# Kernel tuning notes

Measured on AMD Instinct MI355X. Metric: run time of the kernel, lower is better.

## Reference

```python
import jax, jax.numpy as jnp
import numpy as np

EPS = 1e-5

def conv1x1(x, w, b):
    # x: [B,C,H,W], w: [O,C], b: [O]
    return jnp.einsum('oc,bchw->bohw', w, x) + b[None, :, None, None]

def mean_variance_norm(feat):
    # per-(batch,channel) stats over spatial dims; torch.var default is unbiased (ddof=1)
    b, c = feat.shape[:2]
    flat = feat.reshape(b, c, -1)
    mean = jnp.mean(flat, axis=2)[:, :, None, None]
    std = jnp.sqrt(jnp.var(flat, axis=2, ddof=1) + EPS)[:, :, None, None]
    return (feat - mean) / std

def setup_inputs() -> dict:
    key = jax.random.key(0)
    ks = jax.random.split(key, 10)
    B, C, H, W = 4, 256, 64, 64
    sc = 1.0 / np.sqrt(C)
    return {
        'content': jax.random.normal(ks[0], (B, C, H, W), jnp.float32),
        'style': jax.random.normal(ks[1], (B, C, H, W), jnp.float32),
        'content_key': jax.random.normal(ks[2], (B, C, H, W), jnp.float32),
        'style_key': jax.random.normal(ks[3], (B, C, H, W), jnp.float32),
        'f_w': jax.random.normal(ks[4], (C, C), jnp.float32) * sc,
        'f_b': jax.random.normal(ks[5], (C,), jnp.float32) * 0.01,
        'g_w': jax.random.normal(ks[6], (C, C), jnp.float32) * sc,
        'g_b': jax.random.normal(ks[7], (C,), jnp.float32) * 0.01,
        'h_w': jax.random.normal(ks[8], (C, C), jnp.float32) * sc,
        'h_b': jax.random.normal(ks[9], (C,), jnp.float32) * 0.01,
    }

def reference(content, style, content_key, style_key, f_w, f_b, g_w, g_b, h_w, h_b):
    Fq = conv1x1(content_key, f_w, f_b)   # [B,C,Hc,Wc]
    G = conv1x1(style_key, g_w, g_b)      # [B,C,Hs,Ws]
    Hv = conv1x1(style, h_w, h_b)         # [B,C,Hs,Ws]
    b, c, h, w = Fq.shape
    hw_c = h * w
    hw_s = G.shape[2] * G.shape[3]
    Fm = Fq.reshape(b, c, hw_c).transpose(0, 2, 1)       # [B,Nq,C]
    Gm = G.reshape(b, c, hw_s)                            # [B,C,Nk]
    style_flat = Hv.reshape(b, c, hw_s).transpose(0, 2, 1)  # [B,Nk,C]
    S = jax.nn.softmax(jnp.einsum('bqc,bck->bqk', Fm, Gm), axis=-1)  # [B,Nq,Nk]
    mean = jnp.einsum('bqk,bkc->bqc', S, style_flat)
    second = jnp.einsum('bqk,bkc->bqc', S, style_flat ** 2)
    std = jnp.sqrt(jax.nn.relu(second - mean ** 2))
    mean = mean.reshape(b, h, w, c).transpose(0, 3, 1, 2)
    std = std.reshape(b, h, w, c).transpose(0, 3, 1, 2)
    return std * mean_variance_norm(content) + mean
```

## Files before the change

### kernel.cpp

```cpp
#include <hip/hip_runtime.h>
#include <math.h>

#define NSP 4096
#define CD  256
#define LOG2E 1.44269504f

typedef _Float16 half8 __attribute__((ext_vector_type(8)));
typedef _Float16 half4v __attribute__((ext_vector_type(4)));
typedef float f32x4 __attribute__((ext_vector_type(4)));
typedef unsigned int u32;

#define VMCNT(n) asm volatile("s_waitcnt vmcnt(" #n ")" ::: "memory")
#define LGKM0    asm volatile("s_waitcnt lgkmcnt(0)" ::: "memory")

__device__ __forceinline__ void gl16(const void* g, void* l) {
    __builtin_amdgcn_global_load_lds((const __attribute__((address_space(1))) u32*)g,
                                     (__attribute__((address_space(3))) u32*)l, 16, 0, 0);
}

template<int MODE>
__global__ __launch_bounds__(256, 2) void conv_kernel(
    const float* __restrict__ W, const float* __restrict__ bias,
    const float* __restrict__ Xall, _Float16* __restrict__ Yh, _Float16* __restrict__ Yl)
{
    const int b = blockIdx.z;
    const float* X = Xall + (size_t)b * CD * NSP;
    _Float16* Yhb = Yh + (size_t)b * CD * NSP * (MODE == 2 ? 2 : 1);
    _Float16* Ylb = (MODE == 2) ? nullptr : Yl + (size_t)b * CD * NSP;
    __shared__ float Ws[16][128];
    __shared__ float Xs[16][128];
    const int t = threadIdx.x;
    const int tx = t & 15, ty = t >> 4;
    const int m0 = blockIdx.y * 128, n0 = blockIdx.x * 128;
    float acc[8][8];
#pragma unroll
    for (int i = 0; i < 8; ++i)
#pragma unroll
        for (int j = 0; j < 8; ++j) acc[i][j] = 0.f;

    for (int k0 = 0; k0 < CD; k0 += 16) {
        __syncthreads();
        {
            int m = t >> 1, k = (t & 1) * 8;
            float4 w0 = *reinterpret_cast<const float4*>(&W[(size_t)(m0 + m) * CD + k0 + k]);
            float4 w1 = *reinterpret_cast<const float4*>(&W[(size_t)(m0 + m) * CD + k0 + k + 4]);
            Ws[k + 0][m] = w0.x; Ws[k + 1][m] = w0.y; Ws[k + 2][m] = w0.z; Ws[k + 3][m] = w0.w;
            Ws[k + 4][m] = w1.x; Ws[k + 5][m] = w1.y; Ws[k + 6][m] = w1.z; Ws[k + 7][m] = w1.w;
        }
        {
            int k = t >> 4, n = (t & 15) * 8;
            *reinterpret_cast<float4*>(&Xs[k][n]) =
                *reinterpret_cast<const float4*>(&X[(size_t)(k0 + k) * NSP + n0 + n]);
            *reinterpret_cast<float4*>(&Xs[k][n + 4]) =
                *reinterpret_cast<const float4*>(&X[(size_t)(k0 + k) * NSP + n0 + n + 4]);
        }
        __syncthreads();
#pragma unroll
        for (int k = 0; k < 16; ++k) {
            float a[8], bb[8];
            float4 a0 = *reinterpret_cast<const float4*>(&Ws[k][ty * 8]);
            float4 a1 = *reinterpret_cast<const float4*>(&Ws[k][ty * 8 + 4]);
            float4 b0 = *reinterpret_cast<const float4*>(&Xs[k][tx * 4]);
            float4 b1 = *reinterpret_cast<const float4*>(&Xs[k][64 + tx * 4]);
            a[0]=a0.x; a[1]=a0.y; a[2]=a0.z; a[3]=a0.w;
            a[4]=a1.x; a[5]=a1.y; a[6]=a1.z; a[7]=a1.w;
            bb[0]=b0.x; bb[1]=b0.y; bb[2]=b0.z; bb[3]=b0.w;
            bb[4]=b1.x; bb[5]=b1.y; bb[6]=b1.z; bb[7]=b1.w;
#pragma unroll
            for (int i = 0; i < 8; ++i)
#pragma unroll
                for (int j = 0; j < 8; ++j) acc[i][j] = fmaf(a[i], bb[j], acc[i][j]);
        }
    }
    float bv[8];
#pragma unroll
    for (int i = 0; i < 8; ++i) bv[i] = bias[m0 + ty * 8 + i];

    if (MODE == 0) {
#pragma unroll
        for (int jj = 0; jj < 8; ++jj) {
            int n = n0 + ((jj < 4) ? (tx * 4 + jj) : (64 + tx * 4 + (jj - 4)));
            half4v h0, h1, l0, l1;
#pragma unroll
            for (int i = 0; i < 4; ++i) {
                float y0 = (acc[i][jj] + bv[i]) * LOG2E;
                _Float16 hh0 = (_Float16)y0; h0[i] = hh0; l0[i] = (_Float16)(y0 - (float)hh0);
                float y1 = (acc[i + 4][jj] + bv[i + 4]) * LOG2E;
                _Float16 hh1 = (_Float16)y1; h1[i] = hh1; l1[i] = (_Float16)(y1 - (float)hh1);
            }
            size_t off = (size_t)n * CD + m0 + ty * 8;
            *reinterpret_cast<half4v*>(&Yhb[off])     = h0;
            *reinterpret_cast<half4v*>(&Yhb[off + 4]) = h1;
            *reinterpret_cast<half4v*>(&Ylb[off])     = l0;
            *reinterpret_cast<half4v*>(&Ylb[off + 4]) = l1;
        }
    } else if (MODE == 1) {
#pragma unroll
        for (int jj = 0; jj < 8; ++jj) {
            int n = n0 + ((jj < 4) ? (tx * 4 + jj) : (64 + tx * 4 + (jj - 4)));
            int tile = n >> 5, key = n & 31;
            int g = (m0 + ty * 8) >> 3;
            size_t base = (size_t)tile * 8192 + (size_t)key * 256
                        + ((((g * 16)) ^ ((key & 7) << 4)) >> 1);
            half4v h0, h1, l0, l1;
#pragma unroll
            for (int i = 0; i < 4; ++i) {
                float y0 = acc[i][jj] + bv[i];
                _Float16 hh0 = (_Float16)y0; h0[i] = hh0; l0[i] = (_Float16)(y0 - (float)hh0);
                float y1 = acc[i + 4][jj] + bv[i + 4];
                _Float16 hh1 = (_Float16)y1; h1[i] = hh1; l1[i] = (_Float16)(y1 - (float)hh1);
            }
            *reinterpret_cast<half4v*>(&Yhb[base])     = h0;
            *reinterpret_cast<half4v*>(&Yhb[base + 4]) = h1;
            *reinterpret_cast<half4v*>(&Ylb[base])     = l0;
            *reinterpret_cast<half4v*>(&Ylb[base + 4]) = l1;
        }
    } else {
#pragma unroll
        for (int i = 0; i < 8; ++i) {
            int ch = m0 + ty * 8 + i;
            int sw = (ch & 7) << 4;
#pragma unroll
            for (int grp = 0; grp < 2; ++grp) {
                int n = n0 + grp * 64 + tx * 4;
                int tile = n >> 5, kin = n & 31;
                int g4 = kin >> 3, pos0 = kin & 7;
                half4v hv, lv;
#pragma unroll
                for (int j = 0; j < 4; ++j) {
                    float y = acc[i][grp * 4 + j] + bv[i];
                    _Float16 hh = (_Float16)y; hv[j] = hh; lv[j] = (_Float16)(y - (float)hh);
                }
                size_t rowb = (size_t)tile * 16384 + (size_t)ch * 64;
                int bh = (g4 * 16 + pos0 * 2) ^ sw;
                int bl = (64 + g4 * 16 + pos0 * 2) ^ sw;
                *reinterpret_cast<half4v*>(&Yhb[rowb + (bh >> 1)]) = hv;
                *reinterpret_cast<half4v*>(&Yhb[rowb + (bl >> 1)]) = lv;
            }
        }
    }
}

#define KB_OFF 0
#define VB_OFF 65536
#define PB_OFF 131072
#define RM_OFF 139264
#define SMEM_BYTES 139776

__global__ __launch_bounds__(512, 2) void attn_kernel(
    const _Float16* __restrict__ Qh_g, const _Float16* __restrict__ Ql_g,
    const _Float16* __restrict__ Kh_g, const _Float16* __restrict__ Kl_g,
    const _Float16* __restrict__ Vhl_g,
    float* __restrict__ Mout, float* __restrict__ Sout)
{
    extern __shared__ char smem[];
    const int tid = threadIdx.x;
    const int lane = tid & 63;
    const int w = tid >> 6;
    const int g4 = lane >> 4;
    const int l15 = lane & 15;
    const int qf = w & 3;
    const int kf = w >> 2;

    const int bid = blockIdx.x;
    const int b = (bid & 7) >> 1;
    const int qb = ((bid >> 3) << 1) | (bid & 1);
    const int q0 = qb * 64;

    const size_t bNC = (size_t)b * NSP * CD;
    const _Float16* Qhb = Qh_g + bNC;
    const _Float16* Qlb = Ql_g + bNC;
    const _Float16* Khb = Kh_g + bNC;
    const _Float16* Klb = Kl_g + bNC;
    const _Float16* Vb  = Vhl_g + bNC * 2;

    const int qrow = q0 + qf * 16 + l15;
    half8 qh[8], ql[8];
#pragma unroll
    for (int ks = 0; ks < 8; ++ks) {
        qh[ks] = *reinterpret_cast<const half8*>(Qhb + (size_t)qrow * CD + ks * 32 + g4 * 8);
        ql[ks] = *reinterpret_cast<const half8*>(Qlb + (size_t)qrow * CD + ks * 32 + g4 * 8);
    }

    auto stageK = [&](int t, int buf) {
        const _Float16* sh = Khb + (size_t)t * 8192 + w * 1024 + lane * 8;
        const _Float16* sl = Klb + (size_t)t * 8192 + w * 1024 + lane * 8;
        char* d = smem + KB_OFF + buf * 32768 + w * 2048;
        gl16(sh,       d);
        gl16(sh + 512, d + 1024);
        gl16(sl,       d + 16384);
        gl16(sl + 512, d + 16384 + 1024);
    };
    auto stageV = [&](int t, int buf) {
        const _Float16* s = Vb + (size_t)t * 16384 + w * 2048 + lane * 8;
        char* d = smem + VB_OFF + buf * 32768 + w * 4096;
        gl16(s,        d);
        gl16(s + 512,  d + 1024);
        gl16(s + 1024, d + 2048);
        gl16(s + 1536, d + 3072);
    };

    stageK(0, 0); stageV(0, 0); stageK(1, 1); stageV(1, 1);

    f32x4 accM[2][4], accS[2][4];
#pragma unroll
    for (int m = 0; m < 2; ++m)
#pragma unroll
        for (int nf = 0; nf < 4; ++nf) {
            accM[m][nf] = (f32x4){0.f, 0.f, 0.f, 0.f};
            accS[m][nf] = (f32x4){0.f, 0.f, 0.f, 0.f};
        }
    float mrun = -3.0e38f, lrun = 0.f;

    half8 ones8;
#pragma unroll
    for (int e = 0; e < 8; ++e) ones8[e] = (_Float16)1.f;

    const int key = kf * 16 + l15;
    const int ksw = (key & 7) << 4;

    for (int t = 0; t < 128; ++t) {
        const int buf = t & 1;

        if (t < 127) { VMCNT(8); } else { VMCNT(0); }
        LGKM0;
        __builtin_amdgcn_s_barrier();
        __builtin_amdgcn_sched_barrier(0);

        half8 vh8A[2], vl8A[2], wh8A[2], wl8A[2];
#pragma unroll
        for (int m = 0; m < 2; ++m) {
            int ch = w * 32 + m * 16 + l15;
            const char* vrow = smem + VB_OFF + buf * 32768 + ch * 128;
            int sw = (ch & 7) << 4;
            half8 vh8 = *reinterpret_cast<const half8*>(vrow + ((g4 * 16) ^ sw));
            half8 vl8 = *reinterpret_cast<const half8*>(vrow + ((64 + g4 * 16) ^ sw));
            vh8A[m] = vh8; vl8A[m] = vl8;
            half8 wh8, wl8;
#pragma unroll
            for (int e = 0; e < 8; ++e) {
                float v = (float)vh8[e] + (float)vl8[e];
                float wv = v * v;
                _Float16 hh = (_Float16)wv;
                wh8[e] = hh; wl8[e] = (_Float16)(wv - (float)hh);
            }
            wh8A[m] = wh8; wl8A[m] = wl8;
        }

        const char* krow = smem + KB_OFF + buf * 32768 + key * 512;
        f32x4 s = (f32x4){0.f, 0.f, 0.f, 0.f};
        __builtin_amdgcn_s_setprio(1);
#pragma unroll
        for (int ks = 0; ks < 8; ++ks) {
            int off = ((ks * 4 + g4) * 16) ^ ksw;
            half8 bh = *reinterpret_cast<const half8*>(krow + off);
            half8 bl = *reinterpret_cast<const half8*>(krow + 16384 + off);
            s = __builtin_amdgcn_mfma_f32_16x16x32_f16(qh[ks], bh, s, 0, 0, 0);
            s = __builtin_amdgcn_mfma_f32_16x16x32_f16(qh[ks], bl, s, 0, 0, 0);
            s = __builtin_amdgcn_mfma_f32_16x16x32_f16(ql[ks], bh, s, 0, 0, 0);
        }
        __builtin_amdgcn_s_setprio(0);

        f32x4 rmax = s;
#pragma unroll
        for (int mk = 1; mk <= 8; mk <<= 1)
#pragma unroll
            for (int e = 0; e < 4; ++e) rmax[e] = fmaxf(rmax[e], __shfl_xor(rmax[e], mk));
        if (l15 == 0)
            *reinterpret_cast<f32x4*>(smem + RM_OFF + kf * 256 + (qf * 16 + g4 * 4) * 4) = rmax;

        LGKM0;
        __builtin_amdgcn_s_barrier();
        __builtin_amdgcn_sched_barrier(0);

        if (t + 2 < 128) stageK(t + 2, buf);

        const float* rmf = (const float*)(smem + RM_OFF);
        float rm01 = fmaxf(rmf[lane], rmf[64 + lane]);
        bool upd = rm01 > mrun + 8.f;
        float sc = upd ? __builtin_amdgcn_exp2f(mrun - rm01) : 1.f;
        if (upd) mrun = rm01;

#pragma unroll
        for (int e = 0; e < 4; ++e) {
            int q_e = qf * 16 + g4 * 4 + e;
            float m_e = __shfl(mrun, q_e);
            float p = __builtin_amdgcn_exp2f(s[e] - m_e);
            _Float16 hp = (_Float16)p;
            *reinterpret_cast<_Float16*>(smem + PB_OFF + q_e * 128 + ((key * 2) ^ ((q_e & 7) << 4))) = hp;
        }

        if (__ballot(sc < 1.f)) {
#pragma unroll
            for (int nf = 0; nf < 4; ++nf) {
                float scn = __shfl(sc, nf * 16 + l15);
#pragma unroll
                for (int m = 0; m < 2; ++m)
#pragma unroll
                    for (int e = 0; e < 4; ++e) { accM[m][nf][e] *= scn; accS[m][nf][e] *= scn; }
            }
        }

        LGKM0;
        __builtin_amdgcn_s_barrier();
        __builtin_amdgcn_sched_barrier(0);

        half8 pb[4];
#pragma unroll
        for (int nf = 0; nf < 4; ++nf) {
            int q = nf * 16 + l15;
            pb[nf] = *reinterpret_cast<const half8*>(smem + PB_OFF + q * 128 + ((g4 * 16) ^ ((q & 7) << 4)));
        }
        f32x4 po[4];
#pragma unroll
        for (int nf = 0; nf < 4; ++nf) po[nf] = (f32x4){0.f, 0.f, 0.f, 0.f};
        __builtin_amdgcn_s_setprio(1);
#pragma unroll
        for (int nf = 0; nf < 4; ++nf)
            po[nf] = __builtin_amdgcn_mfma_f32_16x16x32_f16(ones8, pb[nf], po[nf], 0, 0, 0);
#pragma unroll
        for (int m = 0; m < 2; ++m) {
#pragma unroll
            for (int nf = 0; nf < 4; ++nf) {
                accM[m][nf] = __builtin_amdgcn_mfma_f32_16x16x32_f16(vh8A[m], pb[nf], accM[m][nf], 0, 0, 0);
                accM[m][nf] = __builtin_amdgcn_mfma_f32_16x16x32_f16(vl8A[m], pb[nf], accM[m][nf], 0, 0, 0);
                accS[m][nf] = __builtin_amdgcn_mfma_f32_16x16x32_f16(wh8A[m], pb[nf], accS[m][nf], 0, 0, 0);
                accS[m][nf] = __builtin_amdgcn_mfma_f32_16x16x32_f16(wl8A[m], pb[nf], accS[m][nf], 0, 0, 0);
            }
        }
        __builtin_amdgcn_s_setprio(0);

        float rsum = (g4 == 0) ? po[0][0] : (g4 == 1) ? po[1][0] : (g4 == 2) ? po[2][0] : po[3][0];
        lrun = lrun * sc + rsum;

        __builtin_amdgcn_sched_barrier(0);
        LGKM0;
        if (t + 2 < 128) stageV(t + 2, buf);
    }

    float inv = 1.f / lrun;
    float linv[4];
#pragma unroll
    for (int nf = 0; nf < 4; ++nf) linv[nf] = __shfl(inv, nf * 16 + l15);

#pragma unroll
    for (int m = 0; m < 2; ++m)
#pragma unroll
        for (int nf = 0; nf < 4; ++nf) {
            int qg = q0 + nf * 16 + l15;
#pragma unroll
            for (int e = 0; e < 4; ++e) {
                int ch = w * 32 + m * 16 + g4 * 4 + e;
                float mean = accM[m][nf][e] * linv[nf];
                float sec  = accS[m][nf][e] * linv[nf];
                float var = sec - mean * mean;
                float sd = sqrtf(fmaxf(var, 0.f));
                size_t off = ((size_t)b * CD + ch) * NSP + qg;
                Mout[off] = mean;
                Sout[off] = sd;
            }
        }
}

__global__ __launch_bounds__(256) void mvn_kernel(
    const float* __restrict__ content, const float* __restrict__ Mn,
    const float* __restrict__ Sd, float* __restrict__ out)
{
    __shared__ float redS[4], redSS[4];
    const int t = threadIdx.x;
    const size_t base = (size_t)blockIdx.x * NSP;
    const float4* x4 = reinterpret_cast<const float4*>(content + base);
    float s = 0.f, ss = 0.f;
    float4 xv[4];
#pragma unroll
    for (int i = 0; i < 4; ++i) {
        float4 v = x4[i * 256 + t];
        xv[i] = v;
        s  += v.x + v.y + v.z + v.w;
        ss += v.x * v.x + v.y * v.y + v.z * v.z + v.w * v.w;
    }
#pragma unroll
    for (int mk = 1; mk < 64; mk <<= 1) { s += __shfl_xor(s, mk); ss += __shfl_xor(ss, mk); }
    if ((t & 63) == 0) { redS[t >> 6] = s; redSS[t >> 6] = ss; }
    __syncthreads();
    float tot   = redS[0] + redS[1] + redS[2] + redS[3];
    float totss = redSS[0] + redSS[1] + redSS[2] + redSS[3];
    float mu  = tot * (1.f / 4096.f);
    float var = (totss - 4096.f * mu * mu) * (1.f / 4095.f);
    float rstd = 1.f / sqrtf(var + 1e-5f);
    const float4* m4 = reinterpret_cast<const float4*>(Mn + base);
    const float4* s4 = reinterpret_cast<const float4*>(Sd + base);
    float4* o4 = reinterpret_cast<float4*>(out + base);
#pragma unroll
    for (int i = 0; i < 4; ++i) {
        float4 mv = m4[i * 256 + t];
        float4 sv = s4[i * 256 + t];
        float4 v  = xv[i];
        float4 o;
        o.x = sv.x * ((v.x - mu) * rstd) + mv.x;
        o.y = sv.y * ((v.y - mu) * rstd) + mv.y;
        o.z = sv.z * ((v.z - mu) * rstd) + mv.z;
        o.w = sv.w * ((v.w - mu) * rstd) + mv.w;
        o4[i * 256 + t] = o;
    }
}

extern "C" void kernel_launch(void* const* d_in, const int* in_sizes, int n_in,
                              void* d_out, int out_size, void* d_ws, size_t ws_size,
                              hipStream_t stream)
{
    const float* content     = (const float*)d_in[0];
    const float* style       = (const float*)d_in[1];
    const float* content_key = (const float*)d_in[2];
    const float* style_key   = (const float*)d_in[3];
    const float* f_w = (const float*)d_in[4];
    const float* f_b = (const float*)d_in[5];
    const float* g_w = (const float*)d_in[6];
    const float* g_b = (const float*)d_in[7];
    const float* h_w = (const float*)d_in[8];
    const float* h_b = (const float*)d_in[9];
    float* out = (float*)d_out;

    const size_t TS = (size_t)4 * NSP * CD;
    _Float16* ws16 = (_Float16*)d_ws;
    _Float16* Qh  = ws16;
    _Float16* Ql  = ws16 + TS;
    _Float16* Kh  = ws16 + 2 * TS;
    _Float16* Kl  = ws16 + 3 * TS;
    _Float16* Vhl = ws16 + 4 * TS;
    float* Mn = (float*)(ws16 + 6 * TS);
    float* Sd = Mn + TS;

    dim3 cgrid(32, 2, 4);
    conv_kernel<0><<<cgrid, 256, 0, stream>>>(f_w, f_b, content_key, Qh, Ql);
    conv_kernel<1><<<cgrid, 256, 0, stream>>>(g_w, g_b, style_key, Kh, Kl);
    conv_kernel<2><<<cgrid, 256, 0, stream>>>(h_w, h_b, style, Vhl, Vhl);
    attn_kernel<<<dim3(256), 512, SMEM_BYTES, stream>>>(Qh, Ql, Kh, Kl, Vhl, Mn, Sd);
    mvn_kernel<<<dim3(1024), 256, 0, stream>>>(content, Mn, Sd, out);
}
```

Baseline: 571.8 us.

## Shrink attention tile to 32 queries, load V directly to registers

```diff
diff --git a/kernel.cpp b/kernel.cpp
--- a/kernel.cpp
+++ b/kernel.cpp
@@ -119,35 +119,33 @@
 #pragma unroll
         for (int i = 0; i < 8; ++i) {
             int ch = m0 + ty * 8 + i;
-            int sw = (ch & 7) << 4;
+            int wv_ = ch >> 6, mv = (ch >> 4) & 3, lv = ch & 15;
+            size_t chbase = (size_t)(wv_ * 8 + mv) * 512 + lv * 8;
 #pragma unroll
             for (int grp = 0; grp < 2; ++grp) {
                 int n = n0 + grp * 64 + tx * 4;
                 int tile = n >> 5, kin = n & 31;
-                int g4 = kin >> 3, pos0 = kin & 7;
-                half4v hv, lv;
+                int g4v = kin >> 3, pos0 = kin & 7;
+                half4v hv, lv4;
 #pragma unroll
                 for (int j = 0; j < 4; ++j) {
                     float y = acc[i][grp * 4 + j] + bv[i];
-                    _Float16 hh = (_Float16)y; hv[j] = hh; lv[j] = (_Float16)(y - (float)hh);
+                    _Float16 hh = (_Float16)y; hv[j] = hh; lv4[j] = (_Float16)(y - (float)hh);
                 }
-                size_t rowb = (size_t)tile * 16384 + (size_t)ch * 64;
-                int bh = (g4 * 16 + pos0 * 2) ^ sw;
-                int bl = (64 + g4 * 16 + pos0 * 2) ^ sw;
-                *reinterpret_cast<half4v*>(&Yhb[rowb + (bh >> 1)]) = hv;
-                *reinterpret_cast<half4v*>(&Yhb[rowb + (bl >> 1)]) = lv;
+                size_t tb = (size_t)tile * 16384 + chbase + (size_t)g4v * 128 + pos0;
+                *reinterpret_cast<half4v*>(&Yhb[tb])        = hv;
+                *reinterpret_cast<half4v*>(&Yhb[tb + 2048]) = lv4;
             }
         }
     }
 }
 
 #define KB_OFF 0
-#define VB_OFF 65536
-#define PB_OFF 131072
-#define RM_OFF 139264
-#define SMEM_BYTES 139776
-
-__global__ __launch_bounds__(512, 2) void attn_kernel(
+#define PB_OFF 65536
+#define RM_OFF 69632
+#define SMEM_BYTES 69888
+
+__global__ __launch_bounds__(256, 2) void attn_kernel(
     const _Float16* __restrict__ Qh_g, const _Float16* __restrict__ Ql_g,
     const _Float16* __restrict__ Kh_g, const _Float16* __restrict__ Kl_g,
     const _Float16* __restrict__ Vhl_g,
@@ -159,13 +157,13 @@
     const int w = tid >> 6;
     const int g4 = lane >> 4;
     const int l15 = lane & 15;
-    const int qf = w & 3;
-    const int kf = w >> 2;
+    const int kf = w & 1;
+    const int qf = w >> 1;
 
     const int bid = blockIdx.x;
     const int b = (bid & 7) >> 1;
     const int qb = ((bid >> 3) << 1) | (bid & 1);
-    const int q0 = qb * 64;
+    const int q0 = qb * 32;
 
     const size_t bNC = (size_t)b * NSP * CD;
     const _Float16* Qhb = Qh_g + bNC;
@@ -183,30 +181,23 @@
     }
 
     auto stageK = [&](int t, int buf) {
-        const _Float16* sh = Khb + (size_t)t * 8192 + w * 1024 + lane * 8;
-        const _Float16* sl = Klb + (size_t)t * 8192 + w * 1024 + lane * 8;
-        char* d = smem + KB_OFF + buf * 32768 + w * 2048;
-        gl16(sh,       d);
-        gl16(sh + 512, d + 1024);
-        gl16(sl,       d + 16384);
-        gl16(sl + 512, d + 16384 + 1024);
+        const _Float16* sh = Khb + (size_t)t * 8192 + tid * 8;
+        const _Float16* sl = Klb + (size_t)t * 8192 + tid * 8;
+        char* d = smem + KB_OFF + buf * 32768 + tid * 16;
+#pragma unroll
+        for (int j = 0; j < 4; ++j) {
+            gl16(sh + j * 2048, d + j * 4096);
+            gl16(sl + j * 2048, d + 16384 + j * 4096);
+        }
     };
-    auto stageV = [&](int t, int buf) {
-        const _Float16* s = Vb + (size_t)t * 16384 + w * 2048 + lane * 8;
-        char* d = smem + VB_OFF + buf * 32768 + w * 4096;
-        gl16(s,        d);
-        gl16(s + 512,  d + 1024);
-        gl16(s + 1024, d + 2048);
-        gl16(s + 1536, d + 3072);
-    };
-
-    stageK(0, 0); stageV(0, 0); stageK(1, 1); stageV(1, 1);
-
-    f32x4 accM[2][4], accS[2][4];
-#pragma unroll
-    for (int m = 0; m < 2; ++m)
-#pragma unroll
-        for (int nf = 0; nf < 4; ++nf) {
+
+    stageK(0, 0); stageK(1, 1);
+
+    f32x4 accM[4][2], accS[4][2];
+#pragma unroll
+    for (int m = 0; m < 4; ++m)
+#pragma unroll
+        for (int nf = 0; nf < 2; ++nf) {
             accM[m][nf] = (f32x4){0.f, 0.f, 0.f, 0.f};
             accS[m][nf] = (f32x4){0.f, 0.f, 0.f, 0.f};
         }
@@ -218,24 +209,101 @@
 
     const int key = kf * 16 + l15;
     const int ksw = (key & 7) << 4;
+    const int qloc = qf * 16 + l15;
+    const int qsw = (qloc & 7) << 4;
+    const size_t vlane = (size_t)g4 * 128 + (size_t)l15 * 8;
+
+    half8 vh[4], vl[4];
 
     for (int t = 0; t < 128; ++t) {
         const int buf = t & 1;
 
-        if (t < 127) { VMCNT(8); } else { VMCNT(0); }
+        if (t <= 126) { VMCNT(8); } else { VMCNT(0); }
         LGKM0;
         __builtin_amdgcn_s_barrier();
         __builtin_amdgcn_sched_barrier(0);
 
-        half8 vh8A[2], vl8A[2], wh8A[2], wl8A[2];
-#pragma unroll
-        for (int m = 0; m < 2; ++m) {
-            int ch = w * 32 + m * 16 + l15;
-            const char* vrow = smem + VB_OFF + buf * 32768 + ch * 128;
-            int sw = (ch & 7) << 4;
-            half8 vh8 = *reinterpret_cast<const half8*>(vrow + ((g4 * 16) ^ sw));
-            half8 vl8 = *reinterpret_cast<const half8*>(vrow + ((64 + g4 * 16) ^ sw));
-            vh8A[m] = vh8; vl8A[m] = vl8;
+        {
+            const _Float16* Vt = Vb + (size_t)t * 16384;
+#pragma unroll
+            for (int m = 0; m < 4; ++m) {
+                vh[m] = *reinterpret_cast<const half8*>(Vt + (size_t)(w * 8 + m) * 512 + vlane);
+                vl[m] = *reinterpret_cast<const half8*>(Vt + (size_t)(w * 8 + 4 + m) * 512 + vlane);
+            }
+        }
+
+        const char* krow = smem + KB_OFF + buf * 32768 + key * 512;
+        f32x4 s = (f32x4){0.f, 0.f, 0.f, 0.f};
+        __builtin_amdgcn_s_setprio(1);
+#pragma unroll
+        for (int ks = 0; ks < 8; ++ks) {
+            int off = ((ks * 4 + g4) * 16) ^ ksw;
+            half8 bh = *reinterpret_cast<const half8*>(krow + off);
+            half8 bl = *reinterpret_cast<const half8*>(krow + 16384 + off);
+            s = __builtin_amdgcn_mfma_f32_16x16x32_f16(bh, qh[ks], s, 0, 0, 0);
+            s = __builtin_amdgcn_mfma_f32_16x16x32_f16(bh, ql[ks], s, 0, 0, 0);
+            s = __builtin_amdgcn_mfma_f32_16x16x32_f16(bl, qh[ks], s, 0, 0, 0);
+        }
+        __builtin_amdgcn_s_setprio(0);
+
+        float rmx = fmaxf(fmaxf(s[0], s[1]), fmaxf(s[2], s[3]));
+        rmx = fmaxf(rmx, __shfl_xor(rmx, 16));
+        rmx = fmaxf(rmx, __shfl_xor(rmx, 32));
+        if (g4 == 0) ((float*)(smem + RM_OFF))[kf * 32 + l15 + qf * 16] = rmx;
+
+        LGKM0;
+        __builtin_amdgcn_s_barrier();
+        __builtin_amdgcn_sched_barrier(0);
+
+        if (t + 2 < 128) stageK(t + 2, buf);
+
+        const float* rmf = (const float*)(smem + RM_OFF);
+        int ql_ = lane & 31;
+        float rm01 = fmaxf(rmf[ql_], rmf[32 + ql_]);
+        bool upd = rm01 > mrun + 8.f;
+        float sc = upd ? __builtin_amdgcn_exp2f(mrun - rm01) : 1.f;
+        if (upd) mrun = rm01;
+
+        float m_q = __shfl(mrun, qloc);
+        half4v hp4;
+#pragma unroll
+        for (int e = 0; e < 4; ++e)
+            hp4[e] = (_Float16)__builtin_amdgcn_exp2f(s[e] - m_q);
+        *reinterpret_cast<half4v*>(smem + PB_OFF + qloc * 128 + ((kf * 32 + g4 * 8) ^ qsw)) = hp4;
+
+        if (__ballot(sc < 1.f)) {
+#pragma unroll
+            for (int nf = 0; nf < 2; ++nf) {
+                float scn = __shfl(sc, nf * 16 + l15);
+#pragma unroll
+                for (int m = 0; m < 4; ++m)
+#pragma unroll
+                    for (int e = 0; e < 4; ++e) { accM[m][nf][e] *= scn; accS[m][nf][e] *= scn; }
+            }
+        }
+
+        LGKM0;
+        __builtin_amdgcn_s_barrier();
+        __builtin_amdgcn_sched_barrier(0);
+
+        if (t <= 125) { VMCNT(8); } else { VMCNT(0); }
+
+        half8 pb[2];
+#pragma unroll
+        for (int nf = 0; nf < 2; ++nf) {
+            int q = nf * 16 + l15;
+            pb[nf] = *reinterpret_cast<const half8*>(smem + PB_OFF + q * 128 + ((g4 * 16) ^ ((q & 7) << 4)));
+        }
+        f32x4 po[2];
+#pragma unroll
+        for (int nf = 0; nf < 2; ++nf) po[nf] = (f32x4){0.f, 0.f, 0.f, 0.f};
+        __builtin_amdgcn_s_setprio(1);
+#pragma unroll
+        for (int nf = 0; nf < 2; ++nf)
+            po[nf] = __builtin_amdgcn_mfma_f32_16x16x32_f16(ones8, pb[nf], po[nf], 0, 0, 0);
+#pragma unroll
+        for (int m = 0; m < 4; ++m) {
+            half8 vh8 = vh[m], vl8 = vl[m];
             half8 wh8, wl8;
 #pragma unroll
             for (int e = 0; e < 8; ++e) {
@@ -244,113 +312,34 @@
                 _Float16 hh = (_Float16)wv;
                 wh8[e] = hh; wl8[e] = (_Float16)(wv - (float)hh);
             }
-            wh8A[m] = wh8; wl8A[m] = wl8;
-        }
-
-        const char* krow = smem + KB_OFF + buf * 32768 + key * 512;
-        f32x4 s = (f32x4){0.f, 0.f, 0.f, 0.f};
-        __builtin_amdgcn_s_setprio(1);
-#pragma unroll
-        for (int ks = 0; ks < 8; ++ks) {
-            int off = ((ks * 4 + g4) * 16) ^ ksw;
-            half8 bh = *reinterpret_cast<const half8*>(krow + off);
-            half8 bl = *reinterpret_cast<const half8*>(krow + 16384 + off);
-            s = __builtin_amdgcn_mfma_f32_16x16x32_f16(qh[ks], bh, s, 0, 0, 0);
-            s = __builtin_amdgcn_mfma_f32_16x16x32_f16(qh[ks], bl, s, 0, 0, 0);
-            s = __builtin_amdgcn_mfma_f32_16x16x32_f16(ql[ks], bh, s, 0, 0, 0);
+#pragma unroll
+            for (int nf = 0; nf < 2; ++nf) {
+                accM[m][nf] = __builtin_amdgcn_mfma_f32_16x16x32_f16(vh8, pb[nf], accM[m][nf], 0, 0, 0);
+                accM[m][nf] = __builtin_amdgcn_mfma_f32_16x16x32_f16(vl8, pb[nf], accM[m][nf], 0, 0, 0);
+                accS[m][nf] = __builtin_amdgcn_mfma_f32_16x16x32_f16(wh8, pb[nf], accS[m][nf], 0, 0, 0);
+                accS[m][nf] = __builtin_amdgcn_mfma_f32_16x16x32_f16(wl8, pb[nf], accS[m][nf], 0, 0, 0);
+            }
         }
         __builtin_amdgcn_s_setprio(0);
 
-        f32x4 rmax = s;
-#pragma unroll
-        for (int mk = 1; mk <= 8; mk <<= 1)
-#pragma unroll
-            for (int e = 0; e < 4; ++e) rmax[e] = fmaxf(rmax[e], __shfl_xor(rmax[e], mk));
-        if (l15 == 0)
-            *reinterpret_cast<f32x4*>(smem + RM_OFF + kf * 256 + (qf * 16 + g4 * 4) * 4) = rmax;
-
-        LGKM0;
-        __builtin_amdgcn_s_barrier();
+        float rsum = (g4 & 1) ? po[1][0] : po[0][0];
+        lrun = lrun * sc + rsum;
         __builtin_amdgcn_sched_barrier(0);
-
-        if (t + 2 < 128) stageK(t + 2, buf);
-
-        const float* rmf = (const float*)(smem + RM_OFF);
-        float rm01 = fmaxf(rmf[lane], rmf[64 + lane]);
-        bool upd = rm01 > mrun + 8.f;
-        float sc = upd ? __builtin_amdgcn_exp2f(mrun - rm01) : 1.f;
-        if (upd) mrun = rm01;
-
-#pragma unroll
-        for (int e = 0; e < 4; ++e) {
-            int q_e = qf * 16 + g4 * 4 + e;
-            float m_e = __shfl(mrun, q_e);
-            float p = __builtin_amdgcn_exp2f(s[e] - m_e);
-            _Float16 hp = (_Float16)p;
-            *reinterpret_cast<_Float16*>(smem + PB_OFF + q_e * 128 + ((key * 2) ^ ((q_e & 7) << 4))) = hp;
-        }
-
-        if (__ballot(sc < 1.f)) {
-#pragma unroll
-            for (int nf = 0; nf < 4; ++nf) {
-                float scn = __shfl(sc, nf * 16 + l15);
-#pragma unroll
-                for (int m = 0; m < 2; ++m)
-#pragma unroll
-                    for (int e = 0; e < 4; ++e) { accM[m][nf][e] *= scn; accS[m][nf][e] *= scn; }
-            }
-        }
-
-        LGKM0;
-        __builtin_amdgcn_s_barrier();
-        __builtin_amdgcn_sched_barrier(0);
-
-        half8 pb[4];
-#pragma unroll
-        for (int nf = 0; nf < 4; ++nf) {
-            int q = nf * 16 + l15;
-            pb[nf] = *reinterpret_cast<const half8*>(smem + PB_OFF + q * 128 + ((g4 * 16) ^ ((q & 7) << 4)));
-        }
-        f32x4 po[4];
-#pragma unroll
-        for (int nf = 0; nf < 4; ++nf) po[nf] = (f32x4){0.f, 0.f, 0.f, 0.f};
-        __builtin_amdgcn_s_setprio(1);
-#pragma unroll
-        for (int nf = 0; nf < 4; ++nf)
-            po[nf] = __builtin_amdgcn_mfma_f32_16x16x32_f16(ones8, pb[nf], po[nf], 0, 0, 0);
-#pragma unroll
-        for (int m = 0; m < 2; ++m) {
-#pragma unroll
-            for (int nf = 0; nf < 4; ++nf) {
-                accM[m][nf] = __builtin_amdgcn_mfma_f32_16x16x32_f16(vh8A[m], pb[nf], accM[m][nf], 0, 0, 0);
-                accM[m][nf] = __builtin_amdgcn_mfma_f32_16x16x32_f16(vl8A[m], pb[nf], accM[m][nf], 0, 0, 0);
-                accS[m][nf] = __builtin_amdgcn_mfma_f32_16x16x32_f16(wh8A[m], pb[nf], accS[m][nf], 0, 0, 0);
-                accS[m][nf] = __builtin_amdgcn_mfma_f32_16x16x32_f16(wl8A[m], pb[nf], accS[m][nf], 0, 0, 0);
-            }
-        }
-        __builtin_amdgcn_s_setprio(0);
-
-        float rsum = (g4 == 0) ? po[0][0] : (g4 == 1) ? po[1][0] : (g4 == 2) ? po[2][0] : po[3][0];
-        lrun = lrun * sc + rsum;
-
-        __builtin_amdgcn_sched_barrier(0);
-        LGKM0;
-        if (t + 2 < 128) stageV(t + 2, buf);
     }
 
     float inv = 1.f / lrun;
-    float linv[4];
-#pragma unroll
-    for (int nf = 0; nf < 4; ++nf) linv[nf] = __shfl(inv, nf * 16 + l15);
-
-#pragma unroll
-    for (int m = 0; m < 2; ++m)
-#pragma unroll
-        for (int nf = 0; nf < 4; ++nf) {
+    float linv[2];
+#pragma unroll
+    for (int nf = 0; nf < 2; ++nf) linv[nf] = __shfl(inv, nf * 16 + l15);
+
+#pragma unroll
+    for (int m = 0; m < 4; ++m)
+#pragma unroll
+        for (int nf = 0; nf < 2; ++nf) {
             int qg = q0 + nf * 16 + l15;
 #pragma unroll
             for (int e = 0; e < 4; ++e) {
-                int ch = w * 32 + m * 16 + g4 * 4 + e;
+                int ch = w * 64 + m * 16 + g4 * 4 + e;
                 float mean = accM[m][nf][e] * linv[nf];
                 float sec  = accS[m][nf][e] * linv[nf];
                 float var = sec - mean * mean;
@@ -435,6 +424,6 @@
     conv_kernel<0><<<cgrid, 256, 0, stream>>>(f_w, f_b, content_key, Qh, Ql);
     conv_kernel<1><<<cgrid, 256, 0, stream>>>(g_w, g_b, style_key, Kh, Kl);
     conv_kernel<2><<<cgrid, 256, 0, stream>>>(h_w, h_b, style, Vhl, Vhl);
-    attn_kernel<<<dim3(256), 512, SMEM_BYTES, stream>>>(Qh, Ql, Kh, Kl, Vhl, Mn, Sd);
+    attn_kernel<<<dim3(512), 256, SMEM_BYTES, stream>>>(Qh, Ql, Kh, Kl, Vhl, Mn, Sd);
     mvn_kernel<<<dim3(1024), 256, 0, stream>>>(content, Mn, Sd, out);
 }
```

After: 566.0 us. About the same (-1.0%).
